# Performance work log

Measured on AMD Instinct MI355X. Metric: run time of the kernel, lower is better.

The kernel has to match this reference:

```python
import jax, jax.numpy as jnp
import numpy as np
from jax import lax

B, C, H, W = 32, 256, 56, 56
K = 3  # kernel_size

def setup_inputs() -> dict:
    key = jax.random.key(0)
    k1, k2, k3 = jax.random.split(key, 3)
    x = jax.random.normal(k1, (B, C, H, W), dtype=jnp.float32)
    # 1x1 conv weight Conv2d(C, C*K*K, 1) flattened to a linear map [C*K*K, C]
    Wk = jax.random.normal(k2, (C * K * K, C), dtype=jnp.float32) * 0.02
    bk = jax.random.normal(k3, (C * K * K,), dtype=jnp.float32) * 0.02
    return {"x": x, "Wk": Wk, "bk": bk}

def reference(x, Wk, bk):
    b, c, h, w = x.shape
    # kernel generator: global avg pool -> 1x1 conv -> relu
    pooled = x.mean(axis=(2, 3))                       # [B, C]
    kern = jax.nn.relu(pooled @ Wk.T + bk)             # [B, C*K*K]
    kern = kern.reshape(b * c, 1, K, K)                # OIHW, one filter per (b,c)
    # per-sample, per-channel depthwise conv: groups = B*C
    xr = x.reshape(1, b * c, h, w)
    out = lax.conv_general_dilated(
        xr, kern,
        window_strides=(1, 1),
        padding=[(K // 2, K // 2), (K // 2, K // 2)],
        feature_group_count=b * c,
        dimension_numbers=("NCHW", "OIHW", "NCHW"),
    )
    return out.reshape(b, c, h, w)
```

## Files before the change

### kernel.cpp

```cpp
#include <hip/hip_runtime.h>

#define B_  32
#define C_  256
#define H_  56
#define W_  56
#define HW  3136
#define KK  9
#define NPLANES (B_*C_)

typedef float v4f __attribute__((ext_vector_type(4)));

__global__ __launch_bounds__(256) void pool_kernel(const float* __restrict__ x,
                                                   float* __restrict__ pooled) {
    const int wid  = threadIdx.x >> 6;
    const int lane = threadIdx.x & 63;
    const int plane = blockIdx.x * 4 + wid;
    const float4* xp = (const float4*)(x + (size_t)plane * HW);

    float s = 0.f;
    #pragma unroll
    for (int k = 0; k < 12; ++k) {
        float4 v = xp[lane + k * 64];
        s += (v.x + v.y) + (v.z + v.w);
    }
    if (lane < 16) {
        float4 v = xp[768 + lane];
        s += (v.x + v.y) + (v.z + v.w);
    }
    #pragma unroll
    for (int off = 32; off > 0; off >>= 1)
        s += __shfl_down(s, off, 64);
    if (lane == 0)
        pooled[plane] = s * (1.0f / (float)HW);
}

__global__ __launch_bounds__(256, 8) void dconv_kernel(const float* __restrict__ x,
                                                       const float* __restrict__ pooled,
                                                       const float* __restrict__ Wk,
                                                       const float* __restrict__ bk,
                                                       float* __restrict__ out) {
    const int plane = blockIdx.x;
    const int b = plane >> 8;
    const int c = plane & 255;
    __shared__ float wsh[KK];
    const int t = threadIdx.x;

    if (t < 144) {
        const int o  = t >> 4;
        const int ch = (t & 15) << 4;
        const int og = c * KK + o;
        const float4* wr = (const float4*)(Wk + (size_t)og * C_ + ch);
        const float4* pr = (const float4*)(pooled + b * C_ + ch);
        float s = 0.f;
        #pragma unroll
        for (int i = 0; i < 4; ++i) {
            float4 w = wr[i];
            float4 p = pr[i];
            s += w.x * p.x + w.y * p.y + w.z * p.z + w.w * p.w;
        }
        #pragma unroll
        for (int off = 8; off > 0; off >>= 1)
            s += __shfl_down(s, off, 16);
        if ((t & 15) == 0)
            wsh[o] = fmaxf(s + bk[og], 0.f);
    }
    __syncthreads();

    const float w0 = wsh[0], w1 = wsh[1], w2 = wsh[2],
                w3 = wsh[3], w4 = wsh[4], w5 = wsh[5],
                w6 = wsh[6], w7 = wsh[7], w8 = wsh[8];

    const float* xp = x + (size_t)plane * HW;
    float* op = out + (size_t)plane * HW;

    const int lane = t & 63;
    const int k    = lane & 15;
    const int g    = lane >> 4;
    const int wv   = t >> 6;
    const bool ka  = (k < 14);
    const int c0   = ka ? (k << 2) : 0;
    const bool hl  = (k > 0);
    const bool hr  = (k < 13);

    #pragma unroll
    for (int half = 0; half < 2; ++half) {
        const int rp = half * 16 + wv * 4 + g;
        if (rp >= 28) break;

        const int rA = (rp == 0)  ? 0  : 2 * rp - 1;
        const int rB = (rp == 27) ? 55 : 2 * rp + 2;

        float4 A  = *(const float4*)(xp + rA * W_ + c0);
        float4 M  = *(const float4*)(xp + (2 * rp) * W_ + c0);
        float4 N  = *(const float4*)(xp + (2 * rp + 1) * W_ + c0);
        float4 Bv = *(const float4*)(xp + rB * W_ + c0);
        if (rp == 0)  { A.x = 0.f;  A.y = 0.f;  A.z = 0.f;  A.w = 0.f; }
        if (rp == 27) { Bv.x = 0.f; Bv.y = 0.f; Bv.z = 0.f; Bv.w = 0.f; }

        if (ka) {
            float Al = __shfl_up(A.w, 1, 16),  Ar = __shfl_down(A.x, 1, 16);
            float Ml = __shfl_up(M.w, 1, 16),  Mr = __shfl_down(M.x, 1, 16);
            float Nl = __shfl_up(N.w, 1, 16),  Nr = __shfl_down(N.x, 1, 16);
            float Bl = __shfl_up(Bv.w, 1, 16), Br = __shfl_down(Bv.x, 1, 16);
            Al = hl ? Al : 0.f;  Ml = hl ? Ml : 0.f;
            Nl = hl ? Nl : 0.f;  Bl = hl ? Bl : 0.f;
            Ar = hr ? Ar : 0.f;  Mr = hr ? Mr : 0.f;
            Nr = hr ? Nr : 0.f;  Br = hr ? Br : 0.f;

            v4f t0, t1;
            t0.x = w0*Al  + w1*A.x  + w2*A.y  + w3*Ml  + w4*M.x  + w5*M.y  + w6*Nl  + w7*N.x  + w8*N.y;
            t0.y = w0*A.x + w1*A.y  + w2*A.z  + w3*M.x + w4*M.y  + w5*M.z  + w6*N.x + w7*N.y  + w8*N.z;
            t0.z = w0*A.y + w1*A.z  + w2*A.w  + w3*M.y + w4*M.z  + w5*M.w  + w6*N.y + w7*N.z  + w8*N.w;
            t0.w = w0*A.z + w1*A.w  + w2*Ar   + w3*M.z + w4*M.w  + w5*Mr   + w6*N.z + w7*N.w  + w8*Nr;
            t1.x = w0*Ml  + w1*M.x  + w2*M.y  + w3*Nl  + w4*N.x  + w5*N.y  + w6*Bl  + w7*Bv.x + w8*Bv.y;
            t1.y = w0*M.x + w1*M.y  + w2*M.z  + w3*N.x + w4*N.y  + w5*N.z  + w6*Bv.x+ w7*Bv.y + w8*Bv.z;
            t1.z = w0*M.y + w1*M.z  + w2*M.w  + w3*N.y + w4*N.z  + w5*N.w  + w6*Bv.y+ w7*Bv.z + w8*Bv.w;
            t1.w = w0*M.z + w1*M.w  + w2*Mr   + w3*N.z + w4*N.w  + w5*Nr   + w6*Bv.z+ w7*Bv.w + w8*Br;

            *(v4f*)(op + (2 * rp + 0) * W_ + c0) = t0;
            *(v4f*)(op + (2 * rp + 1) * W_ + c0) = t1;
        }
    }
}

extern "C" void kernel_launch(void* const* d_in, const int* in_sizes, int n_in,
                              void* d_out, int out_size, void* d_ws, size_t ws_size,
                              hipStream_t stream) {
    const float* x  = (const float*)d_in[0];
    const float* Wk = (const float*)d_in[1];
    const float* bk = (const float*)d_in[2];
    float* out = (float*)d_out;

    float* pooled = (float*)d_ws;

    pool_kernel<<<NPLANES / 4, 256, 0, stream>>>(x, pooled);
    dconv_kernel<<<NPLANES, 256, 0, stream>>>(x, pooled, Wk, bk, out);
}
```

Baseline: 198.5 us.

## Process two planes per block with 8-row register tiles and early loads

The depthwise conv kernel now handles two planes per block. Each thread loads a 10-row column strip into registers and produces 8 output rows, which cuts halo reloads from 2x to 1.25x. The input loads are issued before the per-plane weight GEMV and barrier so memory latency overlaps that computation. Register pressure rises (40 floats of input plus 32 accumulators), so launch bounds drop to 4 blocks and occupancy is lower. Fewer threads do useful work: 14 of 16 row slots are active.

```diff
diff --git a/kernel.cpp b/kernel.cpp
--- a/kernel.cpp
+++ b/kernel.cpp
@@ -34,91 +34,108 @@
         pooled[plane] = s * (1.0f / (float)HW);
 }
 
-__global__ __launch_bounds__(256, 8) void dconv_kernel(const float* __restrict__ x,
+__global__ __launch_bounds__(256, 4) void dconv_kernel(const float* __restrict__ x,
                                                        const float* __restrict__ pooled,
                                                        const float* __restrict__ Wk,
                                                        const float* __restrict__ bk,
                                                        float* __restrict__ out) {
-    const int plane = blockIdx.x;
-    const int b = plane >> 8;
-    const int c = plane & 255;
-    __shared__ float wsh[KK];
-    const int t = threadIdx.x;
-
-    if (t < 144) {
-        const int o  = t >> 4;
-        const int ch = (t & 15) << 4;
-        const int og = c * KK + o;
-        const float4* wr = (const float4*)(Wk + (size_t)og * C_ + ch);
-        const float4* pr = (const float4*)(pooled + b * C_ + ch);
-        float s = 0.f;
-        #pragma unroll
-        for (int i = 0; i < 4; ++i) {
-            float4 w = wr[i];
-            float4 p = pr[i];
-            s += w.x * p.x + w.y * p.y + w.z * p.z + w.w * p.w;
-        }
-        #pragma unroll
-        for (int off = 8; off > 0; off >>= 1)
-            s += __shfl_down(s, off, 16);
-        if ((t & 15) == 0)
-            wsh[o] = fmaxf(s + bk[og], 0.f);
-    }
-    __syncthreads();
-
-    const float w0 = wsh[0], w1 = wsh[1], w2 = wsh[2],
-                w3 = wsh[3], w4 = wsh[4], w5 = wsh[5],
-                w6 = wsh[6], w7 = wsh[7], w8 = wsh[8];
-
-    const float* xp = x + (size_t)plane * HW;
-    float* op = out + (size_t)plane * HW;
+    const int p0 = blockIdx.x * 2;
+    const int t  = threadIdx.x;
+    __shared__ float wsh[2][12];
 
     const int lane = t & 63;
     const int k    = lane & 15;
     const int g    = lane >> 4;
     const int wv   = t >> 6;
-    const bool ka  = (k < 14);
-    const int c0   = ka ? (k << 2) : 0;
-    const bool hl  = (k > 0);
-    const bool hr  = (k < 13);
+    const int s    = wv * 4 + g;
+    const int sp   = (s < 14) ? s : 13;
+    const int pl   = sp / 7;
+    const int rq   = sp % 7;
+    const int kc   = (k < 14) ? k : 13;
+    const int c0   = kc << 2;
+    const bool act = (s < 14) && (k < 14);
+    const int plane = p0 + pl;
+    const float* xp = x + (size_t)plane * HW;
 
+    float4 m[10];
     #pragma unroll
-    for (int half = 0; half < 2; ++half) {
-        const int rp = half * 16 + wv * 4 + g;
-        if (rp >= 28) break;
+    for (int j = 0; j < 10; ++j) {
+        int rr = rq * 8 - 1 + j;
+        rr = rr < 0 ? 0 : (rr > 55 ? 55 : rr);
+        m[j] = *(const float4*)(xp + rr * W_ + c0);
+    }
+    if (rq == 0) { m[0].x = 0.f; m[0].y = 0.f; m[0].z = 0.f; m[0].w = 0.f; }
+    if (rq == 6) { m[9].x = 0.f; m[9].y = 0.f; m[9].z = 0.f; m[9].w = 0.f; }
 
-        const int rA = (rp == 0)  ? 0  : 2 * rp - 1;
-        const int rB = (rp == 27) ? 55 : 2 * rp + 2;
+    if (t < 144) {
+        const int q  = t / 72;
+        const int r  = t % 72;
+        const int o  = r >> 3;
+        const int ch = (r & 7) << 5;
+        const int c  = (p0 + q) & 255;
+        const int b  = p0 >> 8;
+        const int og = c * KK + o;
+        const float4* wr = (const float4*)(Wk + (size_t)og * C_ + ch);
+        const float4* pr = (const float4*)(pooled + b * C_ + ch);
+        float sv = 0.f;
+        #pragma unroll
+        for (int i = 0; i < 8; ++i) {
+            float4 w = wr[i], p = pr[i];
+            sv += w.x * p.x + w.y * p.y + w.z * p.z + w.w * p.w;
+        }
+        sv += __shfl_down(sv, 4, 8);
+        sv += __shfl_down(sv, 2, 8);
+        sv += __shfl_down(sv, 1, 8);
+        if ((r & 7) == 0)
+            wsh[q][o] = fmaxf(sv + bk[og], 0.f);
+    }
+    __syncthreads();
 
-        float4 A  = *(const float4*)(xp + rA * W_ + c0);
-        float4 M  = *(const float4*)(xp + (2 * rp) * W_ + c0);
-        float4 N  = *(const float4*)(xp + (2 * rp + 1) * W_ + c0);
-        float4 Bv = *(const float4*)(xp + rB * W_ + c0);
-        if (rp == 0)  { A.x = 0.f;  A.y = 0.f;  A.z = 0.f;  A.w = 0.f; }
-        if (rp == 27) { Bv.x = 0.f; Bv.y = 0.f; Bv.z = 0.f; Bv.w = 0.f; }
+    const float w0 = wsh[pl][0], w1 = wsh[pl][1], w2 = wsh[pl][2],
+                w3 = wsh[pl][3], w4 = wsh[pl][4], w5 = wsh[pl][5],
+                w6 = wsh[pl][6], w7 = wsh[pl][7], w8 = wsh[pl][8];
 
-        if (ka) {
-            float Al = __shfl_up(A.w, 1, 16),  Ar = __shfl_down(A.x, 1, 16);
-            float Ml = __shfl_up(M.w, 1, 16),  Mr = __shfl_down(M.x, 1, 16);
-            float Nl = __shfl_up(N.w, 1, 16),  Nr = __shfl_down(N.x, 1, 16);
-            float Bl = __shfl_up(Bv.w, 1, 16), Br = __shfl_down(Bv.x, 1, 16);
-            Al = hl ? Al : 0.f;  Ml = hl ? Ml : 0.f;
-            Nl = hl ? Nl : 0.f;  Bl = hl ? Bl : 0.f;
-            Ar = hr ? Ar : 0.f;  Mr = hr ? Mr : 0.f;
-            Nr = hr ? Nr : 0.f;  Br = hr ? Br : 0.f;
+    float acc[8][4];
+    #pragma unroll
+    for (int o = 0; o < 8; ++o) {
+        acc[o][0] = 0.f; acc[o][1] = 0.f; acc[o][2] = 0.f; acc[o][3] = 0.f;
+    }
+    #pragma unroll
+    for (int j = 0; j < 10; ++j) {
+        const float4 mm = m[j];
+        float ml = __shfl_up(mm.w, 1, 16);
+        float mr = __shfl_down(mm.x, 1, 16);
+        if (k == 0)  ml = 0.f;
+        if (k >= 13) mr = 0.f;
+        const float n0 = ml, n1 = mm.x, n2 = mm.y, n3 = mm.z, n4 = mm.w, n5 = mr;
 
-            v4f t0, t1;
-            t0.x = w0*Al  + w1*A.x  + w2*A.y  + w3*Ml  + w4*M.x  + w5*M.y  + w6*Nl  + w7*N.x  + w8*N.y;
-            t0.y = w0*A.x + w1*A.y  + w2*A.z  + w3*M.x + w4*M.y  + w5*M.z  + w6*N.x + w7*N.y  + w8*N.z;
-            t0.z = w0*A.y + w1*A.z  + w2*A.w  + w3*M.y + w4*M.z  + w5*M.w  + w6*N.y + w7*N.z  + w8*N.w;
-            t0.w = w0*A.z + w1*A.w  + w2*Ar   + w3*M.z + w4*M.w  + w5*Mr   + w6*N.z + w7*N.w  + w8*Nr;
-            t1.x = w0*Ml  + w1*M.x  + w2*M.y  + w3*Nl  + w4*N.x  + w5*N.y  + w6*Bl  + w7*Bv.x + w8*Bv.y;
-            t1.y = w0*M.x + w1*M.y  + w2*M.z  + w3*N.x + w4*N.y  + w5*N.z  + w6*Bv.x+ w7*Bv.y + w8*Bv.z;
-            t1.z = w0*M.y + w1*M.z  + w2*M.w  + w3*N.y + w4*N.z  + w5*N.w  + w6*Bv.y+ w7*Bv.z + w8*Bv.w;
-            t1.w = w0*M.z + w1*M.w  + w2*Mr   + w3*N.z + w4*N.w  + w5*Nr   + w6*Bv.z+ w7*Bv.w + w8*Br;
+        if (j < 8) {
+            acc[j][0] += w0*n0 + w1*n1 + w2*n2;
+            acc[j][1] += w0*n1 + w1*n2 + w2*n3;
+            acc[j][2] += w0*n2 + w1*n3 + w2*n4;
+            acc[j][3] += w0*n3 + w1*n4 + w2*n5;
+        }
+        if (j >= 1 && j <= 8) {
+            acc[j-1][0] += w3*n0 + w4*n1 + w5*n2;
+            acc[j-1][1] += w3*n1 + w4*n2 + w5*n3;
+            acc[j-1][2] += w3*n2 + w4*n3 + w5*n4;
+            acc[j-1][3] += w3*n3 + w4*n4 + w5*n5;
+        }
+        if (j >= 2) {
+            acc[j-2][0] += w6*n0 + w7*n1 + w8*n2;
+            acc[j-2][1] += w6*n1 + w7*n2 + w8*n3;
+            acc[j-2][2] += w6*n2 + w7*n3 + w8*n4;
+            acc[j-2][3] += w6*n3 + w7*n4 + w8*n5;
+        }
+    }
 
-            *(v4f*)(op + (2 * rp + 0) * W_ + c0) = t0;
-            *(v4f*)(op + (2 * rp + 1) * W_ + c0) = t1;
+    if (act) {
+        float* op = out + (size_t)plane * HW + (rq * 8) * W_ + c0;
+        #pragma unroll
+        for (int o = 0; o < 8; ++o) {
+            v4f v;
+            v.x = acc[o][0]; v.y = acc[o][1]; v.z = acc[o][2]; v.w = acc[o][3];
+            *(v4f*)(op + o * W_) = v;
         }
     }
 }
@@ -134,5 +151,5 @@
     float* pooled = (float*)d_ws;
 
     pool_kernel<<<NPLANES / 4, 256, 0, stream>>>(x, pooled);
-    dconv_kernel<<<NPLANES, 256, 0, stream>>>(x, pooled, Wk, bk, out);
+    dconv_kernel<<<NPLANES / 2, 256, 0, stream>>>(x, pooled, Wk, bk, out);
 }
```

Result: slower. 204.3 us (+2.9%).

## Fuse pooling and depthwise conv into one kernel with per-batch spin barrier

Applied to the files above, without the earlier changes.

Replaces the separate pool and conv launches with a single kernel in which each block pools its 4 planes, publishes the partial means, and waits on a per-batch atomic counter until all 64 blocks of that batch have arrived. It then computes the generated 3x3 filters for its 4 planes and runs the depthwise conv, reading the planes again while they are likely still in cache. This removes one kernel launch and aims to serve the second read of x from L2 or MALL instead of HBM. In exchange it adds a memset launch and spin-waiting, and it relies on all blocks of a batch being co-resident, which risks deadlock or stalls if scheduling does not guarantee that.

```diff
diff --git a/kernel.cpp b/kernel.cpp
--- a/kernel.cpp
+++ b/kernel.cpp
@@ -6,119 +6,142 @@
 #define W_  56
 #define HW  3136
 #define KK  9
+#define NPB 4
 #define NPLANES (B_*C_)
+#define GRID2 (NPLANES/NPB)
+#define BPB 64
 
 typedef float v4f __attribute__((ext_vector_type(4)));
 
-__global__ __launch_bounds__(256) void pool_kernel(const float* __restrict__ x,
-                                                   float* __restrict__ pooled) {
-    const int wid  = threadIdx.x >> 6;
-    const int lane = threadIdx.x & 63;
-    const int plane = blockIdx.x * 4 + wid;
-    const float4* xp = (const float4*)(x + (size_t)plane * HW);
+__global__ __launch_bounds__(256, 8)
+void fused_kernel(const float* __restrict__ x,
+                  const float* __restrict__ Wk,
+                  const float* __restrict__ bk,
+                  float* __restrict__ pp,
+                  int* __restrict__ bc,
+                  float* __restrict__ out) {
+    __shared__ float psh[C_];
+    __shared__ float wsh[NPB][12];
 
-    float s = 0.f;
-    #pragma unroll
-    for (int k = 0; k < 12; ++k) {
-        float4 v = xp[lane + k * 64];
-        s += (v.x + v.y) + (v.z + v.w);
-    }
-    if (lane < 16) {
-        float4 v = xp[768 + lane];
-        s += (v.x + v.y) + (v.z + v.w);
-    }
-    #pragma unroll
-    for (int off = 32; off > 0; off >>= 1)
-        s += __shfl_down(s, off, 64);
-    if (lane == 0)
-        pooled[plane] = s * (1.0f / (float)HW);
-}
+    const int t    = threadIdx.x;
+    const int lane = t & 63;
+    const int wv   = t >> 6;
+    const int g    = blockIdx.x;
+    const int p0   = g * NPB;
+    const int b    = g >> 6;
 
-__global__ __launch_bounds__(256, 8) void dconv_kernel(const float* __restrict__ x,
-                                                       const float* __restrict__ pooled,
-                                                       const float* __restrict__ Wk,
-                                                       const float* __restrict__ bk,
-                                                       float* __restrict__ out) {
-    const int plane = blockIdx.x;
-    const int b = plane >> 8;
-    const int c = plane & 255;
-    __shared__ float wsh[KK];
-    const int t = threadIdx.x;
-
-    if (t < 144) {
-        const int o  = t >> 4;
-        const int ch = (t & 15) << 4;
-        const int og = c * KK + o;
-        const float4* wr = (const float4*)(Wk + (size_t)og * C_ + ch);
-        const float4* pr = (const float4*)(pooled + b * C_ + ch);
+    {
+        const float4* xp = (const float4*)(x + (size_t)(p0 + wv) * HW);
         float s = 0.f;
         #pragma unroll
-        for (int i = 0; i < 4; ++i) {
-            float4 w = wr[i];
-            float4 p = pr[i];
-            s += w.x * p.x + w.y * p.y + w.z * p.z + w.w * p.w;
+        for (int kk = 0; kk < 12; ++kk) {
+            float4 v = xp[lane + kk * 64];
+            s += (v.x + v.y) + (v.z + v.w);
+        }
+        if (lane < 16) {
+            float4 v = xp[768 + lane];
+            s += (v.x + v.y) + (v.z + v.w);
         }
         #pragma unroll
-        for (int off = 8; off > 0; off >>= 1)
-            s += __shfl_down(s, off, 16);
-        if ((t & 15) == 0)
-            wsh[o] = fmaxf(s + bk[og], 0.f);
+        for (int off = 32; off > 0; off >>= 1)
+            s += __shfl_down(s, off, 64);
+        if (lane == 0)
+            __hip_atomic_store(&pp[(size_t)g * 16 + wv], s * (1.0f / (float)HW),
+                               __ATOMIC_RELAXED, __HIP_MEMORY_SCOPE_AGENT);
+    }
+    __syncthreads();
+    if (t == 0)
+        __hip_atomic_fetch_add(&bc[b * 32], 1, __ATOMIC_ACQ_REL,
+                               __HIP_MEMORY_SCOPE_AGENT);
+
+    if (t == 0) {
+        while (__hip_atomic_load(&bc[b * 32], __ATOMIC_ACQUIRE,
+                                 __HIP_MEMORY_SCOPE_AGENT) < BPB)
+            __builtin_amdgcn_s_sleep(2);
     }
     __syncthreads();
 
-    const float w0 = wsh[0], w1 = wsh[1], w2 = wsh[2],
-                w3 = wsh[3], w4 = wsh[4], w5 = wsh[5],
-                w6 = wsh[6], w7 = wsh[7], w8 = wsh[8];
+    {
+        const int c   = t;
+        const int gp  = (b << 6) + (c >> 2);
+        psh[c] = __hip_atomic_load(&pp[(size_t)gp * 16 + (c & 3)],
+                                   __ATOMIC_RELAXED, __HIP_MEMORY_SCOPE_AGENT);
+    }
+    __syncthreads();
 
-    const float* xp = x + (size_t)plane * HW;
-    float* op = out + (size_t)plane * HW;
+    if (t < 144) {
+        const int j = t >> 2, l = t & 3;
+        const int q = j / KK, o = j % KK;
+        const int c = (p0 + q) & 255;
+        const int og = c * KK + o;
+        const float4* wr  = (const float4*)(Wk + (size_t)og * C_ + l * 64);
+        const float4* pr4 = (const float4*)(psh + l * 64);
+        float sv = 0.f;
+        #pragma unroll 4
+        for (int i = 0; i < 16; ++i) {
+            float4 w = wr[i], p = pr4[i];
+            sv += w.x * p.x + w.y * p.y + w.z * p.z + w.w * p.w;
+        }
+        sv += __shfl_down(sv, 2, 4);
+        sv += __shfl_down(sv, 1, 4);
+        if (l == 0)
+            wsh[q][o] = fmaxf(sv + bk[og], 0.f);
+    }
+    __syncthreads();
 
-    const int lane = t & 63;
-    const int k    = lane & 15;
-    const int g    = lane >> 4;
-    const int wv   = t >> 6;
-    const bool ka  = (k < 14);
-    const int c0   = ka ? (k << 2) : 0;
-    const bool hl  = (k > 0);
-    const bool hr  = (k < 13);
+    const int k   = lane & 15;
+    const int gg  = lane >> 4;
+    const bool ka = (k < 14);
+    const int c0  = ka ? (k << 2) : 0;
+    const bool hl = (k > 0);
+    const bool hr = (k < 13);
 
     #pragma unroll
-    for (int half = 0; half < 2; ++half) {
-        const int rp = half * 16 + wv * 4 + g;
-        if (rp >= 28) break;
+    for (int q = 0; q < NPB; ++q) {
+        const float w0 = wsh[q][0], w1 = wsh[q][1], w2 = wsh[q][2],
+                    w3 = wsh[q][3], w4 = wsh[q][4], w5 = wsh[q][5],
+                    w6 = wsh[q][6], w7 = wsh[q][7], w8 = wsh[q][8];
+        const float* xp = x   + (size_t)(p0 + q) * HW;
+        float*       op = out + (size_t)(p0 + q) * HW;
 
-        const int rA = (rp == 0)  ? 0  : 2 * rp - 1;
-        const int rB = (rp == 27) ? 55 : 2 * rp + 2;
+        #pragma unroll
+        for (int half = 0; half < 2; ++half) {
+            const int rp = half * 16 + wv * 4 + gg;
+            if (rp >= 28) break;
 
-        float4 A  = *(const float4*)(xp + rA * W_ + c0);
-        float4 M  = *(const float4*)(xp + (2 * rp) * W_ + c0);
-        float4 N  = *(const float4*)(xp + (2 * rp + 1) * W_ + c0);
-        float4 Bv = *(const float4*)(xp + rB * W_ + c0);
-        if (rp == 0)  { A.x = 0.f;  A.y = 0.f;  A.z = 0.f;  A.w = 0.f; }
-        if (rp == 27) { Bv.x = 0.f; Bv.y = 0.f; Bv.z = 0.f; Bv.w = 0.f; }
+            const int rA = (rp == 0)  ? 0  : 2 * rp - 1;
+            const int rB = (rp == 27) ? 55 : 2 * rp + 2;
 
-        if (ka) {
-            float Al = __shfl_up(A.w, 1, 16),  Ar = __shfl_down(A.x, 1, 16);
-            float Ml = __shfl_up(M.w, 1, 16),  Mr = __shfl_down(M.x, 1, 16);
-            float Nl = __shfl_up(N.w, 1, 16),  Nr = __shfl_down(N.x, 1, 16);
-            float Bl = __shfl_up(Bv.w, 1, 16), Br = __shfl_down(Bv.x, 1, 16);
-            Al = hl ? Al : 0.f;  Ml = hl ? Ml : 0.f;
-            Nl = hl ? Nl : 0.f;  Bl = hl ? Bl : 0.f;
-            Ar = hr ? Ar : 0.f;  Mr = hr ? Mr : 0.f;
-            Nr = hr ? Nr : 0.f;  Br = hr ? Br : 0.f;
+            float4 A  = *(const float4*)(xp + rA * W_ + c0);
+            float4 M  = *(const float4*)(xp + (2 * rp) * W_ + c0);
+            float4 N  = *(const float4*)(xp + (2 * rp + 1) * W_ + c0);
+            float4 Bv = *(const float4*)(xp + rB * W_ + c0);
+            if (rp == 0)  { A.x = 0.f;  A.y = 0.f;  A.z = 0.f;  A.w = 0.f; }
+            if (rp == 27) { Bv.x = 0.f; Bv.y = 0.f; Bv.z = 0.f; Bv.w = 0.f; }
 
-            v4f t0, t1;
-            t0.x = w0*Al  + w1*A.x  + w2*A.y  + w3*Ml  + w4*M.x  + w5*M.y  + w6*Nl  + w7*N.x  + w8*N.y;
-            t0.y = w0*A.x + w1*A.y  + w2*A.z  + w3*M.x + w4*M.y  + w5*M.z  + w6*N.x + w7*N.y  + w8*N.z;
-            t0.z = w0*A.y + w1*A.z  + w2*A.w  + w3*M.y + w4*M.z  + w5*M.w  + w6*N.y + w7*N.z  + w8*N.w;
-            t0.w = w0*A.z + w1*A.w  + w2*Ar   + w3*M.z + w4*M.w  + w5*Mr   + w6*N.z + w7*N.w  + w8*Nr;
-            t1.x = w0*Ml  + w1*M.x  + w2*M.y  + w3*Nl  + w4*N.x  + w5*N.y  + w6*Bl  + w7*Bv.x + w8*Bv.y;
-            t1.y = w0*M.x + w1*M.y  + w2*M.z  + w3*N.x + w4*N.y  + w5*N.z  + w6*Bv.x+ w7*Bv.y + w8*Bv.z;
-            t1.z = w0*M.y + w1*M.z  + w2*M.w  + w3*N.y + w4*N.z  + w5*N.w  + w6*Bv.y+ w7*Bv.z + w8*Bv.w;
-            t1.w = w0*M.z + w1*M.w  + w2*Mr   + w3*N.z + w4*N.w  + w5*Nr   + w6*Bv.z+ w7*Bv.w + w8*Br;
+            if (ka) {
+                float Al = __shfl_up(A.w, 1, 16),  Ar = __shfl_down(A.x, 1, 16);
+                float Ml = __shfl_up(M.w, 1, 16),  Mr = __shfl_down(M.x, 1, 16);
+                float Nl = __shfl_up(N.w, 1, 16),  Nr = __shfl_down(N.x, 1, 16);
+                float Bl = __shfl_up(Bv.w, 1, 16), Br = __shfl_down(Bv.x, 1, 16);
+                Al = hl ? Al : 0.f;  Ml = hl ? Ml : 0.f;
+                Nl = hl ? Nl : 0.f;  Bl = hl ? Bl : 0.f;
+                Ar = hr ? Ar : 0.f;  Mr = hr ? Mr : 0.f;
+                Nr = hr ? Nr : 0.f;  Br = hr ? Br : 0.f;
 
-            *(v4f*)(op + (2 * rp + 0) * W_ + c0) = t0;
-            *(v4f*)(op + (2 * rp + 1) * W_ + c0) = t1;
+                v4f t0, t1;
+                t0.x = w0*Al  + w1*A.x  + w2*A.y  + w3*Ml  + w4*M.x  + w5*M.y  + w6*Nl  + w7*N.x  + w8*N.y;
+                t0.y = w0*A.x + w1*A.y  + w2*A.z  + w3*M.x + w4*M.y  + w5*M.z  + w6*N.x + w7*N.y  + w8*N.z;
+                t0.z = w0*A.y + w1*A.z  + w2*A.w  + w3*M.y + w4*M.z  + w5*M.w  + w6*N.y + w7*N.z  + w8*N.w;
+                t0.w = w0*A.z + w1*A.w  + w2*Ar   + w3*M.z + w4*M.w  + w5*Mr   + w6*N.z + w7*N.w  + w8*Nr;
+                t1.x = w0*Ml  + w1*M.x  + w2*M.y  + w3*Nl  + w4*N.x  + w5*N.y  + w6*Bl  + w7*Bv.x + w8*Bv.y;
+                t1.y = w0*M.x + w1*M.y  + w2*M.z  + w3*N.x + w4*N.y  + w5*N.z  + w6*Bv.x+ w7*Bv.y + w8*Bv.z;
+                t1.z = w0*M.y + w1*M.z  + w2*M.w  + w3*N.y + w4*N.z  + w5*N.w  + w6*Bv.y+ w7*Bv.z + w8*Bv.w;
+                t1.w = w0*M.z + w1*M.w  + w2*Mr   + w3*N.z + w4*N.w  + w5*Nr   + w6*Bv.z+ w7*Bv.w + w8*Br;
+
+                *(v4f*)(op + (2 * rp + 0) * W_ + c0) = t0;
+                *(v4f*)(op + (2 * rp + 1) * W_ + c0) = t1;
+            }
         }
     }
 }
@@ -131,8 +154,10 @@
     const float* bk = (const float*)d_in[2];
     float* out = (float*)d_out;
 
-    float* pooled = (float*)d_ws;
+    float* pp = (float*)d_ws;
+    int*   bc = (int*)((char*)d_ws + 131072);
 
-    pool_kernel<<<NPLANES / 4, 256, 0, stream>>>(x, pooled);
-    dconv_kernel<<<NPLANES, 256, 0, stream>>>(x, pooled, Wk, bk, out);
+    hipMemsetAsync((char*)d_ws + 131072, 0, 32 * 32 * sizeof(int), stream);
+
+    fused_kernel<<<dim3(GRID2), dim3(256), 0, stream>>>(x, Wk, bk, pp, bc, out);
 }
```

New measurement: 331.3 us. +66.9%, slower.
